# Kernel tuning notes

Measured on AMD Instinct MI355X. Metric: run time of the kernel, lower is better.

Reference implementation:

```python
import jax, jax.numpy as jnp
import numpy as np

B, T_IN, T_OUT, ADIM, PDIM, EDIM = 32, 512, 2048, 384, 4, 1


def setup_inputs() -> dict:
    key = jax.random.key(0)
    ks = jax.random.split(key, 8)
    hs = jax.random.normal(ks[0], (B, T_IN, ADIM), dtype=jnp.float32)
    # durations in [1, 5) so max expanded length 4*T_IN == T_OUT (no truncation)
    durations = jax.random.randint(ks[1], (B, T_IN), 1, 5).astype(jnp.int64)
    input_lengths = (T_IN // 2 + jax.random.randint(ks[2], (B,), 0, T_IN // 2)).astype(jnp.int64)
    pitch_target = jax.random.normal(ks[3], (B, T_OUT, PDIM), dtype=jnp.float32)
    energy_target = jax.random.normal(ks[4], (B, T_OUT, EDIM), dtype=jnp.float32)
    duration_mask = jnp.zeros((B, T_IN, 1), dtype=bool)
    variance_mask = jnp.zeros((B, T_OUT, 1), dtype=bool)
    # kernel-size-1 ConvNorm weights (kernel dim squeezed) + biases
    pitch_w = jax.random.normal(ks[5], (ADIM, PDIM), dtype=jnp.float32) / np.sqrt(PDIM)
    pitch_b = jnp.zeros((ADIM,), dtype=jnp.float32)
    energy_w = jax.random.normal(ks[6], (ADIM, EDIM), dtype=jnp.float32) / np.sqrt(EDIM)
    energy_b = jnp.zeros((ADIM,), dtype=jnp.float32)
    return dict(hs=hs, durations=durations, input_lengths=input_lengths,
                pitch_target=pitch_target, energy_target=energy_target,
                duration_mask=duration_mask, variance_mask=variance_mask,
                pitch_w=pitch_w, pitch_b=pitch_b, energy_w=energy_w, energy_b=energy_b)


def length_regulate(xs, durations, input_lengths, t_out):
    # xs: [B, T_in, D]; durations: [B, T_in]; output: [B, t_out, D], zero-padded
    Bsz, Tin, D = xs.shape
    pos = jnp.arange(Tin)
    valid = pos[None, :] < input_lengths[:, None]            # [B, T_in]
    d = jnp.where(valid, durations, 0)
    total = d.sum(axis=-1)
    # torch: if d.sum()==0, fill truncated d with ones
    d = jnp.where((total == 0)[:, None] & valid, 1, d)
    cum = jnp.cumsum(d, axis=-1)                             # [B, T_in]
    t = jnp.arange(t_out)
    # source phone index per output frame: count of cum entries <= t
    idx = jax.vmap(lambda c: jnp.searchsorted(c, t, side='right'))(cum)  # [B, t_out]
    idx = jnp.clip(idx, 0, Tin - 1)
    out = jnp.take_along_axis(xs, idx[..., None], axis=1)    # [B, t_out, D]
    frame_mask = t[None, :] < cum[:, -1:]                    # [B, t_out]
    return jnp.where(frame_mask[..., None], out, jnp.zeros((), xs.dtype))


def reference(hs, durations, input_lengths, pitch_target, energy_target,
              duration_mask, variance_mask, pitch_w, pitch_b, energy_w, energy_b):
    hs = length_regulate(hs, durations, input_lengths, T_OUT)      # [B, T_out, adim]
    # kernel-size-1 convs == pointwise linear over channel dim (dropout rate 0)
    pitch_embed = jnp.einsum('btp,ap->bta', pitch_target, pitch_w) + pitch_b
    energy_embed = jnp.einsum('bte,ae->bta', energy_target, energy_w) + energy_b
    return hs + pitch_embed + energy_embed
```

## Files before the change

kernel.cpp:

```cpp
#include <hip/hip_runtime.h>

constexpr int kB    = 32;
constexpr int kTin  = 512;
constexpr int kTout = 2048;
constexpr int kA    = 384;
constexpr int kC4   = kA / 4;

constexpr int kBlocksPerBatch = 16;
constexpr int kRowsPerBlock   = kTout / kBlocksPerBatch;

typedef float v4f __attribute__((ext_vector_type(4)));

__global__ __launch_bounds__(384) void va_fused_kernel(
    const float* __restrict__ hs,
    const int*   __restrict__ durations,
    const int*   __restrict__ input_lengths,
    const v4f*   __restrict__ pitch_t,
    const float* __restrict__ energy_t,
    const v4f*   __restrict__ pitch_w,
    const float* __restrict__ pitch_b,
    const float* __restrict__ energy_w,
    const float* __restrict__ energy_b,
    v4f*         __restrict__ out)
{
    __shared__ int bufA[kTin];
    __shared__ int bufB[kTin];

    const int tid = threadIdx.x;
    const int b   = blockIdx.x >> 4;
    const int blk = blockIdx.x & 15;
    const int len = input_lengths[b];

    for (int i = tid; i < kTin; i += 384)
        bufA[i] = (i < len) ? durations[b * kTin + i] : 0;
    __syncthreads();
    int* scur = bufA;
    int* snxt = bufB;
    for (int off = 1; off < kTin; off <<= 1) {
        for (int i = tid; i < kTin; i += 384) {
            int v = scur[i];
            if (i >= off) v += scur[i - off];
            snxt[i] = v;
        }
        __syncthreads();
        int* t = scur; scur = snxt; snxt = t;
    }
    int total = scur[kTin - 1];
    if (total == 0) {
        __syncthreads();
        for (int i = tid; i < kTin; i += 384)
            scur[i] = (i < len) ? 1 : 0;
        __syncthreads();
        for (int off = 1; off < kTin; off <<= 1) {
            for (int i = tid; i < kTin; i += 384) {
                int v = scur[i];
                if (i >= off) v += scur[i - off];
                snxt[i] = v;
            }
            __syncthreads();
            int* t = scur; scur = snxt; snxt = t;
        }
        total = scur[kTin - 1];
    }
    const int* __restrict__ cum = scur;

    const int c4  = tid % kC4;
    const int sub = tid / kC4;
    const int a0  = c4 * 4;

    const v4f w0 = pitch_w[a0];
    const v4f w1 = pitch_w[a0 + 1];
    const v4f w2 = pitch_w[a0 + 2];
    const v4f w3 = pitch_w[a0 + 3];
    v4f ew;
    ew.x = energy_w[a0];     ew.y = energy_w[a0 + 1];
    ew.z = energy_w[a0 + 2]; ew.w = energy_w[a0 + 3];
    v4f bias;
    bias.x = pitch_b[a0]     + energy_b[a0];
    bias.y = pitch_b[a0 + 1] + energy_b[a0 + 1];
    bias.z = pitch_b[a0 + 2] + energy_b[a0 + 2];
    bias.w = pitch_b[a0 + 3] + energy_b[a0 + 3];

    const int row0 = blk * kRowsPerBlock;
    const int hs_base = b * kTin * kA;
    const int row_base = b * kTout;

    for (int r = sub; r < kRowsPerBlock; r += 4) {
        const int to  = row0 + r;
        const int row = row_base + to;

        v4f h = (v4f)(0.f);
        if (to < total) {
            int lo = 0, hi = kTin;
            while (lo < hi) {
                const int mid = (lo + hi) >> 1;
                if (cum[mid] <= to) lo = mid + 1; else hi = mid;
            }
            const int sidx = (lo < kTin) ? lo : (kTin - 1);
            h = *(const v4f*)(hs + hs_base + sidx * kA + a0);
        }
        const v4f  pt = pitch_t[row];
        const float e = energy_t[row];
        v4f o;
        o.x = h.x + pt.x * w0.x + pt.y * w0.y + pt.z * w0.z + pt.w * w0.w + e * ew.x + bias.x;
        o.y = h.y + pt.x * w1.x + pt.y * w1.y + pt.z * w1.z + pt.w * w1.w + e * ew.y + bias.y;
        o.z = h.z + pt.x * w2.x + pt.y * w2.y + pt.z * w2.z + pt.w * w2.w + e * ew.z + bias.z;
        o.w = h.w + pt.x * w3.x + pt.y * w3.y + pt.z * w3.z + pt.w * w3.w + e * ew.w + bias.w;
        __builtin_nontemporal_store(o, &out[row * kC4 + c4]);
    }
}

extern "C" void kernel_launch(void* const* d_in, const int* in_sizes, int n_in,
                              void* d_out, int out_size, void* d_ws, size_t ws_size,
                              hipStream_t stream) {
    const float* hs            = (const float*)d_in[0];
    const int*   durations     = (const int*)d_in[1];
    const int*   input_lengths = (const int*)d_in[2];
    const float* pitch_t       = (const float*)d_in[3];
    const float* energy_t      = (const float*)d_in[4];
    const float* pitch_w       = (const float*)d_in[7];
    const float* pitch_b       = (const float*)d_in[8];
    const float* energy_w      = (const float*)d_in[9];
    const float* energy_b      = (const float*)d_in[10];
    float* out = (float*)d_out;

    va_fused_kernel<<<kB * kBlocksPerBatch, 384, 0, stream>>>(
        hs, durations, input_lengths,
        (const v4f*)pitch_t, energy_t,
        (const v4f*)pitch_w, pitch_b, energy_w, energy_b,
        (v4f*)out);
}
```

Measured before the change: 176.9 us.

## Split length-regulation index computation into a separate per-batch kernel

Moves the cumulative-sum scan and the per-frame binary search into a small kernel that runs once per batch item and writes the source indices to the workspace. Previously each of the 16 blocks per batch redid the scan, and every thread ran its own binary search. The embed kernel now just reads one index per row. It also switches the pitch and energy loads to nontemporal loads. The cost is a second kernel launch and a global round trip for the index array.

```diff
diff --git a/kernel.cpp b/kernel.cpp
--- a/kernel.cpp
+++ b/kernel.cpp
@@ -11,10 +11,47 @@
 
 typedef float v4f __attribute__((ext_vector_type(4)));
 
-__global__ __launch_bounds__(384) void va_fused_kernel(
+__global__ __launch_bounds__(kTin) void lr_index_kernel(
+    const int* __restrict__ durations,
+    const int* __restrict__ input_lengths,
+    int* __restrict__ idx_out)
+{
+    __shared__ int cum[kTin];
+    const int b = blockIdx.x;
+    const int t = threadIdx.x;
+    const int len = input_lengths[b];
+    const bool valid = t < len;
+    int dval = valid ? durations[b * kTin + t] : 0;
+    int total = 0;
+    for (int pass = 0; pass < 2; ++pass) {
+        __syncthreads();
+        cum[t] = dval;
+        __syncthreads();
+        for (int off = 1; off < kTin; off <<= 1) {
+            int add = (t >= off) ? cum[t - off] : 0;
+            __syncthreads();
+            cum[t] += add;
+            __syncthreads();
+        }
+        total = cum[kTin - 1];
+        if (total != 0) break;
+        dval = valid ? 1 : 0;
+    }
+    for (int k = 0; k < kTout / kTin; ++k) {
+        const int to = t + k * kTin;
+        int lo = 0, hi = kTin;
+        while (lo < hi) {
+            const int mid = (lo + hi) >> 1;
+            if (cum[mid] <= to) lo = mid + 1; else hi = mid;
+        }
+        int idx = (lo < kTin) ? lo : (kTin - 1);
+        idx_out[b * kTout + to] = (to < total) ? idx : -1;
+    }
+}
+
+__global__ __launch_bounds__(384) void va_embed_kernel(
     const float* __restrict__ hs,
-    const int*   __restrict__ durations,
-    const int*   __restrict__ input_lengths,
+    const int*   __restrict__ idx,
     const v4f*   __restrict__ pitch_t,
     const float* __restrict__ energy_t,
     const v4f*   __restrict__ pitch_w,
@@ -23,50 +60,13 @@
     const float* __restrict__ energy_b,
     v4f*         __restrict__ out)
 {
-    __shared__ int bufA[kTin];
-    __shared__ int bufB[kTin];
-
     const int tid = threadIdx.x;
-    const int b   = blockIdx.x >> 4;
-    const int blk = blockIdx.x & 15;
-    const int len = input_lengths[b];
-
-    for (int i = tid; i < kTin; i += 384)
-        bufA[i] = (i < len) ? durations[b * kTin + i] : 0;
-    __syncthreads();
-    int* scur = bufA;
-    int* snxt = bufB;
-    for (int off = 1; off < kTin; off <<= 1) {
-        for (int i = tid; i < kTin; i += 384) {
-            int v = scur[i];
-            if (i >= off) v += scur[i - off];
-            snxt[i] = v;
-        }
-        __syncthreads();
-        int* t = scur; scur = snxt; snxt = t;
-    }
-    int total = scur[kTin - 1];
-    if (total == 0) {
-        __syncthreads();
-        for (int i = tid; i < kTin; i += 384)
-            scur[i] = (i < len) ? 1 : 0;
-        __syncthreads();
-        for (int off = 1; off < kTin; off <<= 1) {
-            for (int i = tid; i < kTin; i += 384) {
-                int v = scur[i];
-                if (i >= off) v += scur[i - off];
-                snxt[i] = v;
-            }
-            __syncthreads();
-            int* t = scur; scur = snxt; snxt = t;
-        }
-        total = scur[kTin - 1];
-    }
-    const int* __restrict__ cum = scur;
-
     const int c4  = tid % kC4;
     const int sub = tid / kC4;
     const int a0  = c4 * 4;
+
+    const int b   = blockIdx.x >> 4;
+    const int blk = blockIdx.x & 15;
 
     const v4f w0 = pitch_w[a0];
     const v4f w1 = pitch_w[a0 + 1];
@@ -81,26 +81,20 @@
     bias.z = pitch_b[a0 + 2] + energy_b[a0 + 2];
     bias.w = pitch_b[a0 + 3] + energy_b[a0 + 3];
 
-    const int row0 = blk * kRowsPerBlock;
-    const int hs_base = b * kTin * kA;
+    const int row0     = blk * kRowsPerBlock;
+    const int hs_base  = b * kTin * kA;
     const int row_base = b * kTout;
 
     for (int r = sub; r < kRowsPerBlock; r += 4) {
-        const int to  = row0 + r;
-        const int row = row_base + to;
+        const int row = row_base + row0 + r;
 
+        const int sidx = idx[row];
         v4f h = (v4f)(0.f);
-        if (to < total) {
-            int lo = 0, hi = kTin;
-            while (lo < hi) {
-                const int mid = (lo + hi) >> 1;
-                if (cum[mid] <= to) lo = mid + 1; else hi = mid;
-            }
-            const int sidx = (lo < kTin) ? lo : (kTin - 1);
+        if (sidx >= 0)
             h = *(const v4f*)(hs + hs_base + sidx * kA + a0);
-        }
-        const v4f  pt = pitch_t[row];
-        const float e = energy_t[row];
+
+        const v4f  pt = __builtin_nontemporal_load(&pitch_t[row]);
+        const float e = __builtin_nontemporal_load(&energy_t[row]);
         v4f o;
         o.x = h.x + pt.x * w0.x + pt.y * w0.y + pt.z * w0.z + pt.w * w0.w + e * ew.x + bias.x;
         o.y = h.y + pt.x * w1.x + pt.y * w1.y + pt.z * w1.z + pt.w * w1.w + e * ew.y + bias.y;
@@ -123,9 +117,11 @@
     const float* energy_w      = (const float*)d_in[9];
     const float* energy_b      = (const float*)d_in[10];
     float* out = (float*)d_out;
+    int*   idx = (int*)d_ws;
 
-    va_fused_kernel<<<kB * kBlocksPerBatch, 384, 0, stream>>>(
-        hs, durations, input_lengths,
+    lr_index_kernel<<<kB, kTin, 0, stream>>>(durations, input_lengths, idx);
+    va_embed_kernel<<<kB * kBlocksPerBatch, 384, 0, stream>>>(
+        hs, idx,
         (const v4f*)pitch_t, energy_t,
         (const v4f*)pitch_w, pitch_b, energy_w, energy_b,
         (v4f*)out);
```

Result: slower. 182.1 us (+2.9%).
